# Kernel optimization log

Measured on AMD Instinct MI355X. Metric: run time of the kernel, lower is better.

Reference implementation:

```python
import jax, jax.numpy as jnp
import numpy as np

N = 1048576          # total points
B = 2048             # number of point clouds (segments)
FEAT = 64            # per-point feature dim
ENC = 32             # neighborhood encoder output dim
RADIUS = 1.0


def _linear_params(key, fan_in, fan_out):
    k1, k2 = jax.random.split(key)
    bound = 1.0 / np.sqrt(fan_in)
    w = jax.random.uniform(k1, (fan_in, fan_out), minval=-bound, maxval=bound, dtype=jnp.float32)
    b = jax.random.uniform(k2, (fan_out,), minval=-bound, maxval=bound, dtype=jnp.float32)
    return w, b


def setup_inputs() -> dict:
    key = jax.random.key(0)
    ks = jax.random.split(key, 10)
    points = jax.random.normal(ks[0], (N, 3), dtype=jnp.float32)
    features = jax.random.normal(ks[1], (N, FEAT), dtype=jnp.float32)
    batch = jnp.sort(jax.random.randint(ks[2], (N,), 0, B)).astype(jnp.int64)
    w_ne, b_ne = _linear_params(ks[3], 3, ENC)
    w1, b1 = _linear_params(ks[4], ENC + FEAT, 128)
    w2, b2 = _linear_params(ks[5], 128, 128)
    w3, b3 = _linear_params(ks[6], 128, 128)
    wg1, bg1 = _linear_params(ks[7], 128, 128)
    wg2, bg2 = _linear_params(ks[8], 128, 64)
    wg3, bg3 = _linear_params(ks[9], 64, 32)
    return {"points": points, "features": features, "batch": batch,
            "w_ne": w_ne, "b_ne": b_ne,
            "w1": w1, "b1": b1, "w2": w2, "b2": b2, "w3": w3, "b3": b3,
            "wg1": wg1, "bg1": bg1, "wg2": wg2, "bg2": bg2, "wg3": wg3, "bg3": bg3}


def _segment_max(x, batch, num_segments):
    pooled = jax.ops.segment_max(x, batch, num_segments=num_segments, indices_are_sorted=True)
    # guard empty segments (segment_max fills with -inf)
    return jnp.where(jnp.isneginf(pooled), 0.0, pooled)


def reference(points, features, batch, w_ne, b_ne, w1, b1, w2, b2, w3, b3,
              wg1, bg1, wg2, bg2, wg3, bg3):
    relative_points = points / RADIUS                       # [N, 3]
    # neighborhood encoder: per-point Linear+ReLU, then segment max-pool -> [B, ENC]
    enc = jax.nn.relu(relative_points @ w_ne + b_ne)        # [N, ENC]
    rel_encoded = _segment_max(enc, batch, B)               # [B, ENC]
    rel_enc_mapped = rel_encoded[batch]                     # gather -> [N, ENC]
    fc_input = jnp.concatenate([rel_enc_mapped, features], axis=1)  # [N, ENC+FEAT]
    h = jax.nn.relu(fc_input @ w1 + b1)                     # [N, 128]
    h = jax.nn.relu(h @ w2 + b2)                            # [N, 128]
    h = jax.nn.relu(h @ w3 + b3)                            # [N, 128]
    pooled = _segment_max(h, batch, B)                      # [B, 128]
    g = jax.nn.relu(pooled @ wg1 + bg1)                     # [B, 128]
    g = jax.nn.relu(g @ wg2 + bg2)                          # [B, 64]
    g = jax.nn.relu(g @ wg3 + bg3)                          # [B, 32]
    return g
```

## Files before the change

### kernel.cpp

```cpp
#include <hip/hip_runtime.h>
#include <hip/hip_fp16.h>

#define N_PTS 1048576
#define BSEG  2048
#define XSTR  72

typedef _Float16 half8  __attribute__((ext_vector_type(8)));
typedef _Float16 half4  __attribute__((ext_vector_type(4)));
typedef _Float16 half2v __attribute__((ext_vector_type(2)));
typedef float    floatx4 __attribute__((ext_vector_type(4)));

__global__ __launch_bounds__(256) void wconv(const float* __restrict__ w1,
                                             const float* __restrict__ w2,
                                             const float* __restrict__ w3,
                                             _Float16* __restrict__ w1T,
                                             _Float16* __restrict__ w2T,
                                             _Float16* __restrict__ w3T) {
    int idx = blockIdx.x * 256 + threadIdx.x;
    if (idx < 8192) {
        int j = idx >> 6, k = idx & 63;
        w1T[idx] = (_Float16)w1[(32 + k) * 128 + j];
    } else if (idx < 8192 + 16384) {
        int i = idx - 8192; int j = i >> 7, k = i & 127;
        w2T[i] = (_Float16)w2[k * 128 + j];
    } else if (idx < 8192 + 32768) {
        int i = idx - 8192 - 16384; int j = i >> 7, k = i & 127;
        w3T[i] = (_Float16)w3[k * 128 + j];
    }
}

__global__ __launch_bounds__(256) void enc_pool(const float* __restrict__ pts,
                                                const int* __restrict__ batch,
                                                const float* __restrict__ wne,
                                                const float* __restrict__ bne,
                                                const float* __restrict__ w1,
                                                const float* __restrict__ b1,
                                                float* __restrict__ b1p) {
    const int b = blockIdx.x, tid = threadIdx.x;
    __shared__ float swne[96];
    __shared__ float sbne[32];
    __shared__ float red[4][32];
    __shared__ float sEnc[32];
    if (tid < 96) swne[tid] = wne[tid];
    if (tid < 32) sbne[tid] = bne[tid];

    int lo = 0, hi = N_PTS;
    while (lo < hi) { int mid = (lo + hi) >> 1; if (batch[mid] < b) lo = mid + 1; else hi = mid; }
    const int start = lo;
    hi = N_PTS;
    while (lo < hi) { int mid = (lo + hi) >> 1; if (batch[mid] < b + 1) lo = mid + 1; else hi = mid; }
    const int end = lo;
    __syncthreads();

    float mx[32];
#pragma unroll
    for (int j = 0; j < 32; j++) mx[j] = 0.f;
    for (int p = start + tid; p < end; p += 256) {
        float x0 = pts[3 * p], x1 = pts[3 * p + 1], x2 = pts[3 * p + 2];
#pragma unroll
        for (int j = 0; j < 32; j++) {
            float e = fmaf(x0, swne[j], fmaf(x1, swne[32 + j], fmaf(x2, swne[64 + j], sbne[j])));
            mx[j] = fmaxf(mx[j], e);
        }
    }
#pragma unroll
    for (int j = 0; j < 32; j++) {
#pragma unroll
        for (int off = 1; off < 64; off <<= 1)
            mx[j] = fmaxf(mx[j], __shfl_xor(mx[j], off, 64));
    }
    const int wv = tid >> 6;
    if ((tid & 63) == 0) {
#pragma unroll
        for (int j = 0; j < 32; j++) red[wv][j] = mx[j];
    }
    __syncthreads();
    if (tid < 32)
        sEnc[tid] = fmaxf(fmaxf(red[0][tid], red[1][tid]), fmaxf(red[2][tid], red[3][tid]));
    __syncthreads();
    if (tid < 128) {
        float acc = b1[tid];
#pragma unroll 8
        for (int k = 0; k < 32; k++) acc = fmaf(sEnc[k], w1[k * 128 + tid], acc);
        b1p[b * 128 + tid] = acc;
    }
}

__global__ __launch_bounds__(256, 4) void fused_mlp(
    const float* __restrict__ feat, const int* __restrict__ batch,
    const float* __restrict__ b1p_g,
    const _Float16* __restrict__ w1T, const _Float16* __restrict__ w2T,
    const _Float16* __restrict__ w3T,
    const float* __restrict__ b2, const float* __restrict__ b3,
    const float* __restrict__ wg1, const float* __restrict__ bg1,
    const float* __restrict__ wg2, const float* __restrict__ bg2,
    const float* __restrict__ wg3, const float* __restrict__ bg3,
    float* __restrict__ out) {
    __shared__ __attribute__((aligned(16))) _Float16 xf[2][16 * XSTR];
    __shared__ __attribute__((aligned(16))) _Float16 h1s[16 * 128];
    __shared__ __attribute__((aligned(16))) _Float16 h2s[16 * 128];
    __shared__ float pooled[128];
    __shared__ float g1s[128];
    __shared__ float g2s[64];

    const int b = blockIdx.x, tid = threadIdx.x;
    const int lane = tid & 63, jq = tid >> 6;
    const int l15 = lane & 15, quad = lane >> 4;
    const int podd = l15 & 1;

    int lo = 0, hi = N_PTS;
    while (lo < hi) { int mid = (lo + hi) >> 1; if (batch[mid] < b) lo = mid + 1; else hi = mid; }
    const int start = lo;
    hi = N_PTS;
    while (lo < hi) { int mid = (lo + hi) >> 1; if (batch[mid] < b + 1) lo = mid + 1; else hi = mid; }
    const int end = lo;
    const int n = end - start;
    const int niter = (n + 15) >> 4;

    if (tid < 128) pooled[tid] = 0.f;

    const int jc0 = jq * 32 + l15, jc1 = jc0 + 16;
    half8 w1f[2][2], w2f[2][4], w3f[2][4];
#pragma unroll
    for (int ks = 0; ks < 2; ks++) {
        w1f[0][ks] = *(const half8*)(w1T + jc0 * 64 + ks * 32 + quad * 8);
        w1f[1][ks] = *(const half8*)(w1T + jc1 * 64 + ks * 32 + quad * 8);
    }
#pragma unroll
    for (int ks = 0; ks < 4; ks++) {
        w2f[0][ks] = *(const half8*)(w2T + jc0 * 128 + ks * 32 + quad * 8);
        w2f[1][ks] = *(const half8*)(w2T + jc1 * 128 + ks * 32 + quad * 8);
        w3f[0][ks] = *(const half8*)(w3T + jc0 * 128 + ks * 32 + quad * 8);
        w3f[1][ks] = *(const half8*)(w3T + jc1 * 128 + ks * 32 + quad * 8);
    }
    float bb1[2], bb2[2], bb3[2];
    bb1[0] = b1p_g[b * 128 + jc0]; bb1[1] = b1p_g[b * 128 + jc1];
    bb2[0] = b2[jc0]; bb2[1] = b2[jc1];
    bb3[0] = b3[jc0]; bb3[1] = b3[jc1];

    const int srow = tid >> 4, scol = tid & 15;
    floatx4 pf;
    auto issue = [&](int it) {
        int p = start + it * 16 + srow;
        if (p < end) pf = *(const floatx4*)(feat + (size_t)p * 64 + scol * 4);
        else         pf = (floatx4){0.f, 0.f, 0.f, 0.f};
    };
    auto commit = [&](int buf) {
        half4 hv = {(_Float16)pf.x, (_Float16)pf.y, (_Float16)pf.z, (_Float16)pf.w};
        *(half4*)(&xf[buf][srow * XSTR + scol * 4]) = hv;
    };
    auto storeH = [&](_Float16* hbuf, floatx4* acc, float* bb) {
#pragma unroll
        for (int jt = 0; jt < 2; jt++) {
            float v0 = fmaxf(acc[jt][0] + bb[jt], 0.f);
            float v1 = fmaxf(acc[jt][1] + bb[jt], 0.f);
            float v2 = fmaxf(acc[jt][2] + bb[jt], 0.f);
            float v3 = fmaxf(acc[jt][3] + bb[jt], 0.f);
            float s0 = podd ? v0 : v2;
            float s1 = podd ? v1 : v3;
            s0 = __shfl_xor(s0, 1, 64);
            s1 = __shfl_xor(s1, 1, 64);
            float lo0 = podd ? s0 : v0, hi0 = podd ? v2 : s0;
            float lo1 = podd ? s1 : v1, hi1 = podd ? v3 : s1;
            int r0 = quad * 4 + (podd ? 2 : 0);
            int c0 = jq * 32 + jt * 16 + (l15 & ~1);
            int off0 = r0 * 128 + ((((c0 >> 3) ^ r0) & 15) << 3) + (c0 & 7);
            int r1 = r0 + 1;
            int off1 = r1 * 128 + ((((c0 >> 3) ^ r1) & 15) << 3) + (c0 & 7);
            *(half2v*)(&hbuf[off0]) = (half2v){(_Float16)lo0, (_Float16)hi0};
            *(half2v*)(&hbuf[off1]) = (half2v){(_Float16)lo1, (_Float16)hi1};
        }
    };

    if (niter > 0) { issue(0); commit(0); if (niter > 1) issue(1); }
    __syncthreads();

    float vmax[2] = {0.f, 0.f};

    for (int it = 0; it < niter; it++) {
        const int buf = it & 1;
        floatx4 acc[2];

        acc[0] = (floatx4){0.f, 0.f, 0.f, 0.f};
        acc[1] = (floatx4){0.f, 0.f, 0.f, 0.f};
#pragma unroll
        for (int ks = 0; ks < 2; ks++) {
            half8 a = *(const half8*)(&xf[buf][l15 * XSTR + ks * 32 + quad * 8]);
            acc[0] = __builtin_amdgcn_mfma_f32_16x16x32_f16(a, w1f[0][ks], acc[0], 0, 0, 0);
            acc[1] = __builtin_amdgcn_mfma_f32_16x16x32_f16(a, w1f[1][ks], acc[1], 0, 0, 0);
        }
        storeH(h1s, acc, bb1);
        __syncthreads();

        acc[0] = (floatx4){0.f, 0.f, 0.f, 0.f};
        acc[1] = (floatx4){0.f, 0.f, 0.f, 0.f};
#pragma unroll
        for (int ks = 0; ks < 4; ks++) {
            half8 a = *(const half8*)(&h1s[(l15 << 7) + ((((ks * 4 + quad) ^ l15) & 15) << 3)]);
            acc[0] = __builtin_amdgcn_mfma_f32_16x16x32_f16(a, w2f[0][ks], acc[0], 0, 0, 0);
            acc[1] = __builtin_amdgcn_mfma_f32_16x16x32_f16(a, w2f[1][ks], acc[1], 0, 0, 0);
        }
        storeH(h2s, acc, bb2);
        if (it + 1 < niter) { commit(buf ^ 1); if (it + 2 < niter) issue(it + 2); }
        __syncthreads();

        acc[0] = (floatx4){0.f, 0.f, 0.f, 0.f};
        acc[1] = (floatx4){0.f, 0.f, 0.f, 0.f};
#pragma unroll
        for (int ks = 0; ks < 4; ks++) {
            half8 a = *(const half8*)(&h2s[(l15 << 7) + ((((ks * 4 + quad) ^ l15) & 15) << 3)]);
            acc[0] = __builtin_amdgcn_mfma_f32_16x16x32_f16(a, w3f[0][ks], acc[0], 0, 0, 0);
            acc[1] = __builtin_amdgcn_mfma_f32_16x16x32_f16(a, w3f[1][ks], acc[1], 0, 0, 0);
        }
        const int rowbase = it * 16 + quad * 4;
#pragma unroll
        for (int jt = 0; jt < 2; jt++) {
#pragma unroll
            for (int r = 0; r < 4; r++) {
                float v = ((rowbase + r) < n) ? fmaxf(acc[jt][r] + bb3[jt], 0.f) : 0.f;
                vmax[jt] = fmaxf(vmax[jt], v);
            }
        }
    }

#pragma unroll
    for (int jt = 0; jt < 2; jt++) {
        float m = vmax[jt];
        m = fmaxf(m, __shfl_xor(m, 16, 64));
        m = fmaxf(m, __shfl_xor(m, 32, 64));
        if (quad == 0) pooled[jq * 32 + jt * 16 + l15] = m;
    }
    __syncthreads();

    if (tid < 128) {
        float acc = bg1[tid];
#pragma unroll 8
        for (int k = 0; k < 128; k++) acc = fmaf(pooled[k], wg1[k * 128 + tid], acc);
        g1s[tid] = fmaxf(acc, 0.f);
    }
    __syncthreads();
    if (tid < 64) {
        float acc = bg2[tid];
#pragma unroll 8
        for (int k = 0; k < 128; k++) acc = fmaf(g1s[k], wg2[k * 64 + tid], acc);
        g2s[tid] = fmaxf(acc, 0.f);
    }
    __syncthreads();
    if (tid < 32) {
        float acc = bg3[tid];
#pragma unroll 8
        for (int k = 0; k < 64; k++) acc = fmaf(g2s[k], wg3[k * 32 + tid], acc);
        out[b * 32 + tid] = fmaxf(acc, 0.f);
    }
}

extern "C" void kernel_launch(void* const* d_in, const int* in_sizes, int n_in,
                              void* d_out, int out_size, void* d_ws, size_t ws_size,
                              hipStream_t stream) {
    const float* points = (const float*)d_in[0];
    const float* feat   = (const float*)d_in[1];
    const int*   batch  = (const int*)d_in[2];
    const float* w_ne   = (const float*)d_in[3];
    const float* b_ne   = (const float*)d_in[4];
    const float* w1  = (const float*)d_in[5];
    const float* b1  = (const float*)d_in[6];
    const float* w2  = (const float*)d_in[7];
    const float* b2  = (const float*)d_in[8];
    const float* w3  = (const float*)d_in[9];
    const float* b3  = (const float*)d_in[10];
    const float* wg1 = (const float*)d_in[11];
    const float* bg1 = (const float*)d_in[12];
    const float* wg2 = (const float*)d_in[13];
    const float* bg2 = (const float*)d_in[14];
    const float* wg3 = (const float*)d_in[15];
    const float* bg3 = (const float*)d_in[16];
    float* out = (float*)d_out;

    char* ws = (char*)d_ws;
    float*    b1p = (float*)ws;
    _Float16* w1T = (_Float16*)(ws + 1048576);
    _Float16* w2T = (_Float16*)(ws + 1048576 + 16384);
    _Float16* w3T = (_Float16*)(ws + 1048576 + 16384 + 32768);

    wconv<<<160, 256, 0, stream>>>(w1, w2, w3, w1T, w2T, w3T);
    enc_pool<<<BSEG, 256, 0, stream>>>(points, batch, w_ne, b_ne, w1, b1, b1p);
    fused_mlp<<<BSEG, 256, 0, stream>>>(feat, batch, b1p, w1T, w2T, w3T,
                                        b2, b3, wg1, bg1, wg2, bg2, wg3, bg3, out);
}
```

Before: 555.8 us.

## Software-pipeline the three MLP layers across tiles with one barrier per iteration

Restructures the per-segment loop so layer 3 of tile it-2, layer 2 of tile it-1 and layer 1 of tile it all run in the same iteration. h1/h2 are double-buffered and the feature buffer is triple-buffered, so only one __syncthreads is needed per iteration instead of two. This is meant to cut barrier stalls and expose independent MFMA chains for overlap. In exchange it uses more LDS and registers, which is why the occupancy hint drops from 4 to 3 blocks. The shuffle-based paired half2 store is also replaced by plain scalar half stores.

```diff
diff --git a/kernel.cpp b/kernel.cpp
--- a/kernel.cpp
+++ b/kernel.cpp
@@ -7,7 +7,6 @@
 
 typedef _Float16 half8  __attribute__((ext_vector_type(8)));
 typedef _Float16 half4  __attribute__((ext_vector_type(4)));
-typedef _Float16 half2v __attribute__((ext_vector_type(2)));
 typedef float    floatx4 __attribute__((ext_vector_type(4)));
 
 __global__ __launch_bounds__(256) void wconv(const float* __restrict__ w1,
@@ -86,7 +85,7 @@
     }
 }
 
-__global__ __launch_bounds__(256, 4) void fused_mlp(
+__global__ __launch_bounds__(256, 3) void fused_mlp(
     const float* __restrict__ feat, const int* __restrict__ batch,
     const float* __restrict__ b1p_g,
     const _Float16* __restrict__ w1T, const _Float16* __restrict__ w2T,
@@ -96,9 +95,9 @@
     const float* __restrict__ wg2, const float* __restrict__ bg2,
     const float* __restrict__ wg3, const float* __restrict__ bg3,
     float* __restrict__ out) {
-    __shared__ __attribute__((aligned(16))) _Float16 xf[2][16 * XSTR];
-    __shared__ __attribute__((aligned(16))) _Float16 h1s[16 * 128];
-    __shared__ __attribute__((aligned(16))) _Float16 h2s[16 * 128];
+    __shared__ __attribute__((aligned(16))) _Float16 xf[3][16 * XSTR];
+    __shared__ __attribute__((aligned(16))) _Float16 h1s[2][16 * 128];
+    __shared__ __attribute__((aligned(16))) _Float16 h2s[2][16 * 128];
     __shared__ float pooled[128];
     __shared__ float g1s[128];
     __shared__ float g2s[64];
@@ -106,7 +105,6 @@
     const int b = blockIdx.x, tid = threadIdx.x;
     const int lane = tid & 63, jq = tid >> 6;
     const int l15 = lane & 15, quad = lane >> 4;
-    const int podd = l15 & 1;
 
     int lo = 0, hi = N_PTS;
     while (lo < hi) { int mid = (lo + hi) >> 1; if (batch[mid] < b) lo = mid + 1; else hi = mid; }
@@ -117,8 +115,6 @@
     const int n = end - start;
     const int niter = (n + 15) >> 4;
 
-    if (tid < 128) pooled[tid] = 0.f;
-
     const int jc0 = jq * 32 + l15, jc1 = jc0 + 16;
     half8 w1f[2][2], w2f[2][4], w3f[2][4];
 #pragma unroll
@@ -145,82 +141,97 @@
         if (p < end) pf = *(const floatx4*)(feat + (size_t)p * 64 + scol * 4);
         else         pf = (floatx4){0.f, 0.f, 0.f, 0.f};
     };
-    auto commit = [&](int buf) {
+    auto commitSlot = [&](int slot) {
         half4 hv = {(_Float16)pf.x, (_Float16)pf.y, (_Float16)pf.z, (_Float16)pf.w};
-        *(half4*)(&xf[buf][srow * XSTR + scol * 4]) = hv;
+        *(half4*)(&xf[slot][srow * XSTR + scol * 4]) = hv;
     };
     auto storeH = [&](_Float16* hbuf, floatx4* acc, float* bb) {
 #pragma unroll
         for (int jt = 0; jt < 2; jt++) {
-            float v0 = fmaxf(acc[jt][0] + bb[jt], 0.f);
-            float v1 = fmaxf(acc[jt][1] + bb[jt], 0.f);
-            float v2 = fmaxf(acc[jt][2] + bb[jt], 0.f);
-            float v3 = fmaxf(acc[jt][3] + bb[jt], 0.f);
-            float s0 = podd ? v0 : v2;
-            float s1 = podd ? v1 : v3;
-            s0 = __shfl_xor(s0, 1, 64);
-            s1 = __shfl_xor(s1, 1, 64);
-            float lo0 = podd ? s0 : v0, hi0 = podd ? v2 : s0;
-            float lo1 = podd ? s1 : v1, hi1 = podd ? v3 : s1;
-            int r0 = quad * 4 + (podd ? 2 : 0);
-            int c0 = jq * 32 + jt * 16 + (l15 & ~1);
-            int off0 = r0 * 128 + ((((c0 >> 3) ^ r0) & 15) << 3) + (c0 & 7);
-            int r1 = r0 + 1;
-            int off1 = r1 * 128 + ((((c0 >> 3) ^ r1) & 15) << 3) + (c0 & 7);
-            *(half2v*)(&hbuf[off0]) = (half2v){(_Float16)lo0, (_Float16)hi0};
-            *(half2v*)(&hbuf[off1]) = (half2v){(_Float16)lo1, (_Float16)hi1};
+            int c = jq * 32 + jt * 16 + l15;
+#pragma unroll
+            for (int r = 0; r < 4; r++) {
+                int rr = quad * 4 + r;
+                float v = fmaxf(acc[jt][r] + bb[jt], 0.f);
+                hbuf[rr * 128 + ((((c >> 3) ^ rr) & 15) << 3) + (c & 7)] = (_Float16)v;
+            }
         }
     };
 
-    if (niter > 0) { issue(0); commit(0); if (niter > 1) issue(1); }
+    if (niter > 0) { issue(0); commitSlot(0); if (niter > 1) issue(1); }
     __syncthreads();
 
     float vmax[2] = {0.f, 0.f};
 
-    for (int it = 0; it < niter; it++) {
-        const int buf = it & 1;
-        floatx4 acc[2];
-
-        acc[0] = (floatx4){0.f, 0.f, 0.f, 0.f};
-        acc[1] = (floatx4){0.f, 0.f, 0.f, 0.f};
-#pragma unroll
-        for (int ks = 0; ks < 2; ks++) {
-            half8 a = *(const half8*)(&xf[buf][l15 * XSTR + ks * 32 + quad * 8]);
-            acc[0] = __builtin_amdgcn_mfma_f32_16x16x32_f16(a, w1f[0][ks], acc[0], 0, 0, 0);
-            acc[1] = __builtin_amdgcn_mfma_f32_16x16x32_f16(a, w1f[1][ks], acc[1], 0, 0, 0);
-        }
-        storeH(h1s, acc, bb1);
+    for (int it = 0; it < niter + 2; ++it) {
+        const bool doL1 = (it < niter);
+        const bool doL2 = (it >= 1) && (it <= niter);
+        const bool doL3 = (it >= 2);
+
+        half8 a3[4], a2[4], a1[2];
+        if (doL3) {
+            const _Float16* src = h2s[(it - 2) & 1];
+#pragma unroll
+            for (int ks = 0; ks < 4; ks++)
+                a3[ks] = *(const half8*)(&src[(l15 << 7) + ((((ks * 4 + quad) ^ l15) & 15) << 3)]);
+        }
+        if (doL2) {
+            const _Float16* src = h1s[(it - 1) & 1];
+#pragma unroll
+            for (int ks = 0; ks < 4; ks++)
+                a2[ks] = *(const half8*)(&src[(l15 << 7) + ((((ks * 4 + quad) ^ l15) & 15) << 3)]);
+        }
+        if (doL1) {
+            const _Float16* src = xf[it % 3];
+#pragma unroll
+            for (int ks = 0; ks < 2; ks++)
+                a1[ks] = *(const half8*)(&src[l15 * XSTR + ks * 32 + quad * 8]);
+        }
+        if (it + 1 < niter) commitSlot((it + 1) % 3);
+        if (it + 2 < niter) issue(it + 2);
+
+        if (doL3) {
+            floatx4 acc[2];
+            acc[0] = (floatx4){0.f, 0.f, 0.f, 0.f};
+            acc[1] = (floatx4){0.f, 0.f, 0.f, 0.f};
+#pragma unroll
+            for (int ks = 0; ks < 4; ks++) {
+                acc[0] = __builtin_amdgcn_mfma_f32_16x16x32_f16(a3[ks], w3f[0][ks], acc[0], 0, 0, 0);
+                acc[1] = __builtin_amdgcn_mfma_f32_16x16x32_f16(a3[ks], w3f[1][ks], acc[1], 0, 0, 0);
+            }
+            const int rowbase = (it - 2) * 16 + quad * 4;
+#pragma unroll
+            for (int jt = 0; jt < 2; jt++) {
+#pragma unroll
+                for (int r = 0; r < 4; r++) {
+                    float v = ((rowbase + r) < n) ? fmaxf(acc[jt][r] + bb3[jt], 0.f) : 0.f;
+                    vmax[jt] = fmaxf(vmax[jt], v);
+                }
+            }
+        }
+        if (doL2) {
+            floatx4 acc[2];
+            acc[0] = (floatx4){0.f, 0.f, 0.f, 0.f};
+            acc[1] = (floatx4){0.f, 0.f, 0.f, 0.f};
+#pragma unroll
+            for (int ks = 0; ks < 4; ks++) {
+                acc[0] = __builtin_amdgcn_mfma_f32_16x16x32_f16(a2[ks], w2f[0][ks], acc[0], 0, 0, 0);
+                acc[1] = __builtin_amdgcn_mfma_f32_16x16x32_f16(a2[ks], w2f[1][ks], acc[1], 0, 0, 0);
+            }
+            storeH(h2s[(it - 1) & 1], acc, bb2);
+        }
+        if (doL1) {
+            floatx4 acc[2];
+            acc[0] = (floatx4){0.f, 0.f, 0.f, 0.f};
+            acc[1] = (floatx4){0.f, 0.f, 0.f, 0.f};
+#pragma unroll
+            for (int ks = 0; ks < 2; ks++) {
+                acc[0] = __builtin_amdgcn_mfma_f32_16x16x32_f16(a1[ks], w1f[0][ks], acc[0], 0, 0, 0);
+                acc[1] = __builtin_amdgcn_mfma_f32_16x16x32_f16(a1[ks], w1f[1][ks], acc[1], 0, 0, 0);
+            }
+            storeH(h1s[it & 1], acc, bb1);
+        }
         __syncthreads();
-
-        acc[0] = (floatx4){0.f, 0.f, 0.f, 0.f};
-        acc[1] = (floatx4){0.f, 0.f, 0.f, 0.f};
-#pragma unroll
-        for (int ks = 0; ks < 4; ks++) {
-            half8 a = *(const half8*)(&h1s[(l15 << 7) + ((((ks * 4 + quad) ^ l15) & 15) << 3)]);
-            acc[0] = __builtin_amdgcn_mfma_f32_16x16x32_f16(a, w2f[0][ks], acc[0], 0, 0, 0);
-            acc[1] = __builtin_amdgcn_mfma_f32_16x16x32_f16(a, w2f[1][ks], acc[1], 0, 0, 0);
-        }
-        storeH(h2s, acc, bb2);
-        if (it + 1 < niter) { commit(buf ^ 1); if (it + 2 < niter) issue(it + 2); }
-        __syncthreads();
-
-        acc[0] = (floatx4){0.f, 0.f, 0.f, 0.f};
-        acc[1] = (floatx4){0.f, 0.f, 0.f, 0.f};
-#pragma unroll
-        for (int ks = 0; ks < 4; ks++) {
-            half8 a = *(const half8*)(&h2s[(l15 << 7) + ((((ks * 4 + quad) ^ l15) & 15) << 3)]);
-            acc[0] = __builtin_amdgcn_mfma_f32_16x16x32_f16(a, w3f[0][ks], acc[0], 0, 0, 0);
-            acc[1] = __builtin_amdgcn_mfma_f32_16x16x32_f16(a, w3f[1][ks], acc[1], 0, 0, 0);
-        }
-        const int rowbase = it * 16 + quad * 4;
-#pragma unroll
-        for (int jt = 0; jt < 2; jt++) {
-#pragma unroll
-            for (int r = 0; r < 4; r++) {
-                float v = ((rowbase + r) < n) ? fmaxf(acc[jt][r] + bb3[jt], 0.f) : 0.f;
-                vmax[jt] = fmaxf(vmax[jt], v);
-            }
-        }
     }
 
 #pragma unroll
```

Result: slower. 567.8 us (+2.1%).
